# Kernel optimization log

Hardware: AMD Instinct MI355X
Metric: run time of the kernel (lower is better)

The kernel has to match this reference:

```python
import jax, jax.numpy as jnp
import numpy as np

SOFTMAX_SCALE = 0.5  # passed as scalar arg in the original op

def setup_inputs() -> dict:
    key = jax.random.key(0)
    ks = jax.random.split(key, 6)
    B, Sq, H, D, Smax = 8, 1, 32, 128, 4096
    q = jax.random.normal(ks[0], (B, Sq, H, D), dtype=jnp.float32)
    k = jax.random.normal(ks[1], (B, Sq, H, D), dtype=jnp.float32)
    v = jax.random.normal(ks[2], (B, Sq, H, D), dtype=jnp.float32)
    kcache = jax.random.normal(ks[3], (B, Smax, H, D), dtype=jnp.float32)
    vcache = jax.random.normal(ks[4], (B, Smax, H, D), dtype=jnp.float32)
    # current cache occupancy per batch; ensure seqlen + Sq <= Smax
    seqlen = jax.random.randint(ks[5], (B,), 0, Smax - Sq).astype(jnp.int32)
    return {"q": q, "k": k, "v": v, "kcache": kcache, "vcache": vcache, "seqlen": seqlen}

def reference(q, k, v, kcache, vcache, seqlen):
    # Semantics of flash_attn_with_kvcache: append k/v into the cache at
    # offset seqlen[b], then causally attend q over cache[: seqlen[b] + S_new].
    # Causal alignment is bottom-right: query i maps to key position
    # seqlen + S_new - S_q + i.
    B, Sq, H, D = q.shape
    Smax = kcache.shape[1]
    Snew = k.shape[1]
    pos_k = jnp.arange(Smax)          # [Smax]
    pos_q = jnp.arange(Sq)            # [Sq]

    def one_batch(qb, kb, vb, kcb, vcb, sl):
        # qb: [Sq,H,D]; kcb/vcb: [Smax,H,D]; sl: scalar int32
        kc = jax.lax.dynamic_update_slice(kcb, kb, (sl, 0, 0))
        vc = jax.lax.dynamic_update_slice(vcb, vb, (sl, 0, 0))
        scores = jnp.einsum('qhd,khd->hqk', qb, kc) * SOFTMAX_SCALE  # [H,Sq,Smax]
        kmax = sl + Snew - Sq + pos_q                                # [Sq]
        mask = pos_k[None, :] <= kmax[:, None]                       # [Sq,Smax]
        scores = jnp.where(mask[None, :, :], scores, -jnp.inf)
        p = jax.nn.softmax(scores, axis=-1)
        return jnp.einsum('hqk,khd->qhd', p, vc)                     # [Sq,H,D]

    return jax.vmap(one_batch)(q, k, v, kcache, vcache, seqlen)
```

## Files before the change

kernel.cpp:

```cpp
#include <hip/hip_runtime.h>
#include <math.h>

#define B_    8
#define H_    32
#define D_    128
#define SMAX_ 4096
#define SCALE 0.5f

__global__ __launch_bounds__(256, 4)
void attn_partial(const float* __restrict__ q,
                  const float* __restrict__ knew,
                  const float* __restrict__ vnew,
                  const float* __restrict__ kcache,
                  const float* __restrict__ vcache,
                  const int* __restrict__ seqlen,
                  float* __restrict__ ws,
                  float* __restrict__ out,
                  int nsplit, int chunk)
{
    const int blk   = blockIdx.x;
    const int split = blk % nsplit;
    const int bh    = blk / nsplit;
    const int h     = bh & (H_ - 1);
    const int b     = bh / H_;

    const int sl    = seqlen[b];
    const int total = sl + 1;
    const int cs    = split * chunk;
    const int ce    = min(cs + chunk, total);

    const int tid    = threadIdx.x;
    const int lane16 = tid & 15;
    const int gid    = tid >> 4;

    const int qbase = (b * H_ + h) * D_ + lane16 * 8;
    float qf[8];
    {
        float4 q0 = *(const float4*)(q + qbase);
        float4 q1 = *(const float4*)(q + qbase + 4);
        qf[0]=q0.x; qf[1]=q0.y; qf[2]=q0.z; qf[3]=q0.w;
        qf[4]=q1.x; qf[5]=q1.y; qf[6]=q1.z; qf[7]=q1.w;
    }

    float m = -1e30f, l = 0.f;
    float acc[8];
    #pragma unroll
    for (int j = 0; j < 8; ++j) acc[j] = 0.f;

    const size_t cbase = (size_t)b * SMAX_ * (H_ * D_) + (size_t)h * D_ + (size_t)(lane16 * 8);

    for (int p = cs + gid; p < ce; p += 16) {
        const float* kp;
        const float* vp;
        if (p == sl) {
            kp = knew + qbase;
            vp = vnew + qbase;
        } else {
            size_t off = cbase + (size_t)p * (H_ * D_);
            kp = kcache + off;
            vp = vcache + off;
        }
        float4 k0 = *(const float4*)(kp);
        float4 k1 = *(const float4*)(kp + 4);
        float4 v0 = *(const float4*)(vp);
        float4 v1 = *(const float4*)(vp + 4);

        float s = qf[0]*k0.x + qf[1]*k0.y + qf[2]*k0.z + qf[3]*k0.w
                + qf[4]*k1.x + qf[5]*k1.y + qf[6]*k1.z + qf[7]*k1.w;
        s += __shfl_xor(s, 1);
        s += __shfl_xor(s, 2);
        s += __shfl_xor(s, 4);
        s += __shfl_xor(s, 8);
        s *= SCALE;

        float mn = fmaxf(m, s);
        float sc = __expf(m - mn);
        float pr = __expf(s - mn);
        m = mn;
        l = l * sc + pr;
        acc[0] = fmaf(pr, v0.x, acc[0]*sc);
        acc[1] = fmaf(pr, v0.y, acc[1]*sc);
        acc[2] = fmaf(pr, v0.z, acc[2]*sc);
        acc[3] = fmaf(pr, v0.w, acc[3]*sc);
        acc[4] = fmaf(pr, v1.x, acc[4]*sc);
        acc[5] = fmaf(pr, v1.y, acc[5]*sc);
        acc[6] = fmaf(pr, v1.z, acc[6]*sc);
        acc[7] = fmaf(pr, v1.w, acc[7]*sc);
    }

    #pragma unroll
    for (int off = 16; off <= 32; off <<= 1) {
        float m2 = __shfl_xor(m, off);
        float l2 = __shfl_xor(l, off);
        float a2[8];
        #pragma unroll
        for (int j = 0; j < 8; ++j) a2[j] = __shfl_xor(acc[j], off);
        float mn = fmaxf(m, m2);
        float s1 = __expf(m - mn);
        float s2 = __expf(m2 - mn);
        l = l * s1 + l2 * s2;
        #pragma unroll
        for (int j = 0; j < 8; ++j) acc[j] = acc[j]*s1 + a2[j]*s2;
        m = mn;
    }

    __shared__ float sm_m[4];
    __shared__ float sm_l[4];
    __shared__ float sm_acc[4][D_];
    const int w    = tid >> 6;
    const int lane = tid & 63;
    if (lane < 16) {
        if (lane == 0) { sm_m[w] = m; sm_l[w] = l; }
        #pragma unroll
        for (int j = 0; j < 8; ++j) sm_acc[w][lane16*8 + j] = acc[j];
    }
    __syncthreads();

    if (tid < D_) {
        float m0 = sm_m[0], m1 = sm_m[1], m2 = sm_m[2], m3 = sm_m[3];
        float mt = fmaxf(fmaxf(m0, m1), fmaxf(m2, m3));
        float e0 = __expf(m0 - mt), e1 = __expf(m1 - mt);
        float e2 = __expf(m2 - mt), e3 = __expf(m3 - mt);
        float lt = sm_l[0]*e0 + sm_l[1]*e1 + sm_l[2]*e2 + sm_l[3]*e3;
        float a  = sm_acc[0][tid]*e0 + sm_acc[1][tid]*e1
                 + sm_acc[2][tid]*e2 + sm_acc[3][tid]*e3;
        if (nsplit == 1) {
            out[bh * D_ + tid] = a / lt;
        } else {
            float* wsp = ws + (size_t)blk * (D_ + 2);
            if (tid == 0) { wsp[0] = mt; wsp[1] = lt; }
            wsp[2 + tid] = a;
        }
    }
}

__global__ __launch_bounds__(128)
void attn_combine(const float* __restrict__ ws, float* __restrict__ out, int nsplit)
{
    const int bh = blockIdx.x;
    const int d  = threadIdx.x;
    const float* base = ws + (size_t)bh * nsplit * (D_ + 2);

    float mt = -1e30f;
    for (int s = 0; s < nsplit; ++s) mt = fmaxf(mt, base[(size_t)s * (D_ + 2)]);
    float lt = 0.f, a = 0.f;
    for (int s = 0; s < nsplit; ++s) {
        const float* p = base + (size_t)s * (D_ + 2);
        float e = __expf(p[0] - mt);
        lt += p[1] * e;
        a  += p[2 + d] * e;
    }
    out[bh * D_ + d] = a / lt;
}

extern "C" void kernel_launch(void* const* d_in, const int* in_sizes, int n_in,
                              void* d_out, int out_size, void* d_ws, size_t ws_size,
                              hipStream_t stream) {
    const float* q  = (const float*)d_in[0];
    const float* k  = (const float*)d_in[1];
    const float* v  = (const float*)d_in[2];
    const float* kc = (const float*)d_in[3];
    const float* vc = (const float*)d_in[4];
    const int*   sl = (const int*)d_in[5];
    float* out = (float*)d_out;
    float* ws  = (float*)d_ws;

    int nsplit = 16;
    while (nsplit > 1 &&
           (size_t)B_ * H_ * nsplit * (D_ + 2) * sizeof(float) > ws_size) {
        nsplit >>= 1;
    }
    const int chunk = (SMAX_ + nsplit - 1) / nsplit;
    const int nblk  = B_ * H_ * nsplit;

    attn_partial<<<nblk, 256, 0, stream>>>(q, k, v, kc, vc, sl, ws, out, nsplit, chunk);
    if (nsplit > 1) {
        attn_combine<<<B_ * H_, 128, 0, stream>>>(ws, out, nsplit);
    }
}
```

Measured before the change: 140.1 us.

## Map all heads into one block per batch split, processing full contiguous cache rows

Each block now handles one batch and one sequence split across all 32 heads, so each thread reads 16 contiguous floats and a block covers a full contiguous 16KB cache row per position instead of a 512B head slice. The split count rises to 128 with a rewritten combine kernel that uses shuffle reductions and handles empty splits. The main loop is unrolled by two positions with a shared max update, and the new-token branch is hoisted out of the loop. Possible costs are higher register pressure from 16-wide accumulators and a heavier combine pass, and the nsplit==1 direct-output path is removed, so the combine launch always runs.

New measurement: 196.7 us. 40.4% more time.

```diff
diff --git a/kernel.cpp b/kernel.cpp
--- a/kernel.cpp
+++ b/kernel.cpp
@@ -5,7 +5,9 @@
 #define H_    32
 #define D_    128
 #define SMAX_ 4096
+#define HD_   (H_ * D_)
 #define SCALE 0.5f
+#define PSTRIDE (D_ + 2)
 
 __global__ __launch_bounds__(256, 4)
 void attn_partial(const float* __restrict__ q,
@@ -15,142 +17,196 @@
                   const float* __restrict__ vcache,
                   const int* __restrict__ seqlen,
                   float* __restrict__ ws,
-                  float* __restrict__ out,
                   int nsplit, int chunk)
 {
     const int blk   = blockIdx.x;
     const int split = blk % nsplit;
-    const int bh    = blk / nsplit;
-    const int h     = bh & (H_ - 1);
-    const int b     = bh / H_;
+    const int b     = blk / nsplit;
+    const int tid   = threadIdx.x;
+    const int h     = tid >> 3;
+    const int ds    = (tid & 7) * 16;
 
     const int sl    = seqlen[b];
     const int total = sl + 1;
     const int cs    = split * chunk;
     const int ce    = min(cs + chunk, total);
 
-    const int tid    = threadIdx.x;
-    const int lane16 = tid & 15;
-    const int gid    = tid >> 4;
-
-    const int qbase = (b * H_ + h) * D_ + lane16 * 8;
-    float qf[8];
+    float* wsp = ws + (((size_t)b * nsplit + split) * H_ + h) * PSTRIDE;
+
+    if (cs >= ce) {
+        if ((tid & 7) == 0) { wsp[0] = -1e30f; wsp[1] = 0.f; }
+        return;
+    }
+
+    float qf[16];
     {
-        float4 q0 = *(const float4*)(q + qbase);
-        float4 q1 = *(const float4*)(q + qbase + 4);
-        qf[0]=q0.x; qf[1]=q0.y; qf[2]=q0.z; qf[3]=q0.w;
-        qf[4]=q1.x; qf[5]=q1.y; qf[6]=q1.z; qf[7]=q1.w;
+        const float* qp = q + (b * H_ + h) * D_ + ds;
+        float4 t0 = *(const float4*)(qp);
+        float4 t1 = *(const float4*)(qp + 4);
+        float4 t2 = *(const float4*)(qp + 8);
+        float4 t3 = *(const float4*)(qp + 12);
+        qf[0]=t0.x;  qf[1]=t0.y;  qf[2]=t0.z;  qf[3]=t0.w;
+        qf[4]=t1.x;  qf[5]=t1.y;  qf[6]=t1.z;  qf[7]=t1.w;
+        qf[8]=t2.x;  qf[9]=t2.y;  qf[10]=t2.z; qf[11]=t2.w;
+        qf[12]=t3.x; qf[13]=t3.y; qf[14]=t3.z; qf[15]=t3.w;
     }
 
     float m = -1e30f, l = 0.f;
-    float acc[8];
+    float acc[16];
     #pragma unroll
-    for (int j = 0; j < 8; ++j) acc[j] = 0.f;
-
-    const size_t cbase = (size_t)b * SMAX_ * (H_ * D_) + (size_t)h * D_ + (size_t)(lane16 * 8);
-
-    for (int p = cs + gid; p < ce; p += 16) {
-        const float* kp;
-        const float* vp;
-        if (p == sl) {
-            kp = knew + qbase;
-            vp = vnew + qbase;
-        } else {
-            size_t off = cbase + (size_t)p * (H_ * D_);
-            kp = kcache + off;
-            vp = vcache + off;
-        }
-        float4 k0 = *(const float4*)(kp);
-        float4 k1 = *(const float4*)(kp + 4);
-        float4 v0 = *(const float4*)(vp);
-        float4 v1 = *(const float4*)(vp + 4);
-
-        float s = qf[0]*k0.x + qf[1]*k0.y + qf[2]*k0.z + qf[3]*k0.w
-                + qf[4]*k1.x + qf[5]*k1.y + qf[6]*k1.z + qf[7]*k1.w;
-        s += __shfl_xor(s, 1);
-        s += __shfl_xor(s, 2);
-        s += __shfl_xor(s, 4);
-        s += __shfl_xor(s, 8);
-        s *= SCALE;
-
-        float mn = fmaxf(m, s);
-        float sc = __expf(m - mn);
-        float pr = __expf(s - mn);
+    for (int j = 0; j < 16; ++j) acc[j] = 0.f;
+
+    const float* kb = kcache + (size_t)b * SMAX_ * HD_ + tid * 16;
+    const float* vb = vcache + (size_t)b * SMAX_ * HD_ + tid * 16;
+
+#define STEP1(KP, VP) do {                                                    \
+    float4 k0 = *(const float4*)(KP);                                         \
+    float4 k1 = *(const float4*)((KP)+4);                                     \
+    float4 k2 = *(const float4*)((KP)+8);                                     \
+    float4 k3 = *(const float4*)((KP)+12);                                    \
+    float4 v0 = *(const float4*)(VP);                                         \
+    float4 v1 = *(const float4*)((VP)+4);                                     \
+    float4 v2 = *(const float4*)((VP)+8);                                     \
+    float4 v3 = *(const float4*)((VP)+12);                                    \
+    float s = qf[0]*k0.x+qf[1]*k0.y+qf[2]*k0.z+qf[3]*k0.w                     \
+            + qf[4]*k1.x+qf[5]*k1.y+qf[6]*k1.z+qf[7]*k1.w                     \
+            + qf[8]*k2.x+qf[9]*k2.y+qf[10]*k2.z+qf[11]*k2.w                   \
+            + qf[12]*k3.x+qf[13]*k3.y+qf[14]*k3.z+qf[15]*k3.w;                \
+    s += __shfl_xor(s, 1); s += __shfl_xor(s, 2); s += __shfl_xor(s, 4);      \
+    s *= SCALE;                                                               \
+    float mn = fmaxf(m, s);                                                   \
+    float sc = __expf(m - mn);                                                \
+    float pr = __expf(s - mn);                                                \
+    m = mn; l = l * sc + pr;                                                  \
+    acc[0]=fmaf(pr,v0.x,acc[0]*sc);  acc[1]=fmaf(pr,v0.y,acc[1]*sc);          \
+    acc[2]=fmaf(pr,v0.z,acc[2]*sc);  acc[3]=fmaf(pr,v0.w,acc[3]*sc);          \
+    acc[4]=fmaf(pr,v1.x,acc[4]*sc);  acc[5]=fmaf(pr,v1.y,acc[5]*sc);          \
+    acc[6]=fmaf(pr,v1.z,acc[6]*sc);  acc[7]=fmaf(pr,v1.w,acc[7]*sc);          \
+    acc[8]=fmaf(pr,v2.x,acc[8]*sc);  acc[9]=fmaf(pr,v2.y,acc[9]*sc);          \
+    acc[10]=fmaf(pr,v2.z,acc[10]*sc);acc[11]=fmaf(pr,v2.w,acc[11]*sc);        \
+    acc[12]=fmaf(pr,v3.x,acc[12]*sc);acc[13]=fmaf(pr,v3.y,acc[13]*sc);        \
+    acc[14]=fmaf(pr,v3.z,acc[14]*sc);acc[15]=fmaf(pr,v3.w,acc[15]*sc);        \
+} while (0)
+
+    const int pend = min(ce, sl);
+    int p = cs;
+    for (; p + 2 <= pend; p += 2) {
+        const float* kp0 = kb + (size_t)p * HD_;
+        const float* vp0 = vb + (size_t)p * HD_;
+        const float* kp1 = kp0 + HD_;
+        const float* vp1 = vp0 + HD_;
+        float4 a0 = *(const float4*)(kp0);
+        float4 a1 = *(const float4*)(kp0+4);
+        float4 a2 = *(const float4*)(kp0+8);
+        float4 a3 = *(const float4*)(kp0+12);
+        float4 b0 = *(const float4*)(kp1);
+        float4 b1 = *(const float4*)(kp1+4);
+        float4 b2 = *(const float4*)(kp1+8);
+        float4 b3 = *(const float4*)(kp1+12);
+        float4 u0 = *(const float4*)(vp0);
+        float4 u1 = *(const float4*)(vp0+4);
+        float4 u2 = *(const float4*)(vp0+8);
+        float4 u3 = *(const float4*)(vp0+12);
+        float4 w0 = *(const float4*)(vp1);
+        float4 w1 = *(const float4*)(vp1+4);
+        float4 w2 = *(const float4*)(vp1+8);
+        float4 w3 = *(const float4*)(vp1+12);
+
+        float s0 = qf[0]*a0.x+qf[1]*a0.y+qf[2]*a0.z+qf[3]*a0.w
+                 + qf[4]*a1.x+qf[5]*a1.y+qf[6]*a1.z+qf[7]*a1.w
+                 + qf[8]*a2.x+qf[9]*a2.y+qf[10]*a2.z+qf[11]*a2.w
+                 + qf[12]*a3.x+qf[13]*a3.y+qf[14]*a3.z+qf[15]*a3.w;
+        float s1 = qf[0]*b0.x+qf[1]*b0.y+qf[2]*b0.z+qf[3]*b0.w
+                 + qf[4]*b1.x+qf[5]*b1.y+qf[6]*b1.z+qf[7]*b1.w
+                 + qf[8]*b2.x+qf[9]*b2.y+qf[10]*b2.z+qf[11]*b2.w
+                 + qf[12]*b3.x+qf[13]*b3.y+qf[14]*b3.z+qf[15]*b3.w;
+        s0 += __shfl_xor(s0, 1); s0 += __shfl_xor(s0, 2); s0 += __shfl_xor(s0, 4);
+        s1 += __shfl_xor(s1, 1); s1 += __shfl_xor(s1, 2); s1 += __shfl_xor(s1, 4);
+        s0 *= SCALE; s1 *= SCALE;
+
+        float mn  = fmaxf(m, fmaxf(s0, s1));
+        float sc  = __expf(m - mn);
+        float pr0 = __expf(s0 - mn);
+        float pr1 = __expf(s1 - mn);
         m = mn;
-        l = l * sc + pr;
-        acc[0] = fmaf(pr, v0.x, acc[0]*sc);
-        acc[1] = fmaf(pr, v0.y, acc[1]*sc);
-        acc[2] = fmaf(pr, v0.z, acc[2]*sc);
-        acc[3] = fmaf(pr, v0.w, acc[3]*sc);
-        acc[4] = fmaf(pr, v1.x, acc[4]*sc);
-        acc[5] = fmaf(pr, v1.y, acc[5]*sc);
-        acc[6] = fmaf(pr, v1.z, acc[6]*sc);
-        acc[7] = fmaf(pr, v1.w, acc[7]*sc);
-    }
-
-    #pragma unroll
-    for (int off = 16; off <= 32; off <<= 1) {
-        float m2 = __shfl_xor(m, off);
-        float l2 = __shfl_xor(l, off);
-        float a2[8];
-        #pragma unroll
-        for (int j = 0; j < 8; ++j) a2[j] = __shfl_xor(acc[j], off);
-        float mn = fmaxf(m, m2);
-        float s1 = __expf(m - mn);
-        float s2 = __expf(m2 - mn);
-        l = l * s1 + l2 * s2;
-        #pragma unroll
-        for (int j = 0; j < 8; ++j) acc[j] = acc[j]*s1 + a2[j]*s2;
-        m = mn;
-    }
-
-    __shared__ float sm_m[4];
-    __shared__ float sm_l[4];
-    __shared__ float sm_acc[4][D_];
-    const int w    = tid >> 6;
-    const int lane = tid & 63;
-    if (lane < 16) {
-        if (lane == 0) { sm_m[w] = m; sm_l[w] = l; }
-        #pragma unroll
-        for (int j = 0; j < 8; ++j) sm_acc[w][lane16*8 + j] = acc[j];
-    }
-    __syncthreads();
-
-    if (tid < D_) {
-        float m0 = sm_m[0], m1 = sm_m[1], m2 = sm_m[2], m3 = sm_m[3];
-        float mt = fmaxf(fmaxf(m0, m1), fmaxf(m2, m3));
-        float e0 = __expf(m0 - mt), e1 = __expf(m1 - mt);
-        float e2 = __expf(m2 - mt), e3 = __expf(m3 - mt);
-        float lt = sm_l[0]*e0 + sm_l[1]*e1 + sm_l[2]*e2 + sm_l[3]*e3;
-        float a  = sm_acc[0][tid]*e0 + sm_acc[1][tid]*e1
-                 + sm_acc[2][tid]*e2 + sm_acc[3][tid]*e3;
-        if (nsplit == 1) {
-            out[bh * D_ + tid] = a / lt;
-        } else {
-            float* wsp = ws + (size_t)blk * (D_ + 2);
-            if (tid == 0) { wsp[0] = mt; wsp[1] = lt; }
-            wsp[2 + tid] = a;
-        }
-    }
+        l = l * sc + pr0 + pr1;
+        acc[0] = fmaf(pr1,w0.x, fmaf(pr0,u0.x, acc[0] *sc));
+        acc[1] = fmaf(pr1,w0.y, fmaf(pr0,u0.y, acc[1] *sc));
+        acc[2] = fmaf(pr1,w0.z, fmaf(pr0,u0.z, acc[2] *sc));
+        acc[3] = fmaf(pr1,w0.w, fmaf(pr0,u0.w, acc[3] *sc));
+        acc[4] = fmaf(pr1,w1.x, fmaf(pr0,u1.x, acc[4] *sc));
+        acc[5] = fmaf(pr1,w1.y, fmaf(pr0,u1.y, acc[5] *sc));
+        acc[6] = fmaf(pr1,w1.z, fmaf(pr0,u1.z, acc[6] *sc));
+        acc[7] = fmaf(pr1,w1.w, fmaf(pr0,u1.w, acc[7] *sc));
+        acc[8] = fmaf(pr1,w2.x, fmaf(pr0,u2.x, acc[8] *sc));
+        acc[9] = fmaf(pr1,w2.y, fmaf(pr0,u2.y, acc[9] *sc));
+        acc[10]= fmaf(pr1,w2.z, fmaf(pr0,u2.z, acc[10]*sc));
+        acc[11]= fmaf(pr1,w2.w, fmaf(pr0,u2.w, acc[11]*sc));
+        acc[12]= fmaf(pr1,w3.x, fmaf(pr0,u3.x, acc[12]*sc));
+        acc[13]= fmaf(pr1,w3.y, fmaf(pr0,u3.y, acc[13]*sc));
+        acc[14]= fmaf(pr1,w3.z, fmaf(pr0,u3.z, acc[14]*sc));
+        acc[15]= fmaf(pr1,w3.w, fmaf(pr0,u3.w, acc[15]*sc));
+    }
+    for (; p < pend; ++p) {
+        const float* kp = kb + (size_t)p * HD_;
+        const float* vp = vb + (size_t)p * HD_;
+        STEP1(kp, vp);
+    }
+    if (sl >= cs && sl < ce) {
+        const float* kp = knew + (size_t)b * HD_ + tid * 16;
+        const float* vp = vnew + (size_t)b * HD_ + tid * 16;
+        STEP1(kp, vp);
+    }
+#undef STEP1
+
+    if ((tid & 7) == 0) { wsp[0] = m; wsp[1] = l; }
+    float* op = wsp + 2 + ds;
+    *(float4*)(op)      = make_float4(acc[0],  acc[1],  acc[2],  acc[3]);
+    *(float4*)(op + 4)  = make_float4(acc[4],  acc[5],  acc[6],  acc[7]);
+    *(float4*)(op + 8)  = make_float4(acc[8],  acc[9],  acc[10], acc[11]);
+    *(float4*)(op + 12) = make_float4(acc[12], acc[13], acc[14], acc[15]);
 }
 
 __global__ __launch_bounds__(128)
 void attn_combine(const float* __restrict__ ws, float* __restrict__ out, int nsplit)
 {
     const int bh = blockIdx.x;
-    const int d  = threadIdx.x;
-    const float* base = ws + (size_t)bh * nsplit * (D_ + 2);
-
-    float mt = -1e30f;
-    for (int s = 0; s < nsplit; ++s) mt = fmaxf(mt, base[(size_t)s * (D_ + 2)]);
-    float lt = 0.f, a = 0.f;
+    const int b  = bh >> 5;
+    const int h  = bh & (H_ - 1);
+    const int t  = threadIdx.x;
+
+    __shared__ float sm_e[128];
+    __shared__ float sm_w[2];
+
+    float m_s = -1e30f, l_s = 0.f;
+    const float* ps = ws + (((size_t)b * nsplit + t) * H_ + h) * PSTRIDE;
+    if (t < nsplit) { m_s = ps[0]; l_s = ps[1]; }
+
+    float mx = m_s;
+    #pragma unroll
+    for (int off = 1; off < 64; off <<= 1) mx = fmaxf(mx, __shfl_xor(mx, off));
+    if ((t & 63) == 0) sm_w[t >> 6] = mx;
+    __syncthreads();
+    const float mt = fmaxf(sm_w[0], sm_w[1]);
+    __syncthreads();
+
+    const float e = (l_s > 0.f) ? __expf(m_s - mt) : 0.f;
+    sm_e[t] = e;
+    float le = l_s * e;
+    #pragma unroll
+    for (int off = 1; off < 64; off <<= 1) le += __shfl_xor(le, off);
+    if ((t & 63) == 0) sm_w[t >> 6] = le;
+    __syncthreads();
+    const float lt = sm_w[0] + sm_w[1];
+
+    const float* ab = ws + ((size_t)b * nsplit * H_ + h) * PSTRIDE + 2 + t;
+    const size_t sstride = (size_t)H_ * PSTRIDE;
+    float a = 0.f;
+    #pragma unroll 8
     for (int s = 0; s < nsplit; ++s) {
-        const float* p = base + (size_t)s * (D_ + 2);
-        float e = __expf(p[0] - mt);
-        lt += p[1] * e;
-        a  += p[2 + d] * e;
-    }
-    out[bh * D_ + d] = a / lt;
+        a += sm_e[s] * ab[(size_t)s * sstride];
+    }
+    out[bh * D_ + t] = a / lt;
 }
 
 extern "C" void kernel_launch(void* const* d_in, const int* in_sizes, int n_in,
@@ -165,16 +221,13 @@
     float* out = (float*)d_out;
     float* ws  = (float*)d_ws;
 
-    int nsplit = 16;
+    int nsplit = 128;
     while (nsplit > 1 &&
-           (size_t)B_ * H_ * nsplit * (D_ + 2) * sizeof(float) > ws_size) {
+           (size_t)B_ * nsplit * H_ * PSTRIDE * sizeof(float) > ws_size) {
         nsplit >>= 1;
     }
-    const int chunk = (SMAX_ + nsplit - 1) / nsplit;
-    const int nblk  = B_ * H_ * nsplit;
-
-    attn_partial<<<nblk, 256, 0, stream>>>(q, k, v, kc, vc, sl, ws, out, nsplit, chunk);
-    if (nsplit > 1) {
-        attn_combine<<<B_ * H_, 128, 0, stream>>>(ws, out, nsplit);
-    }
+    const int chunk = SMAX_ / nsplit;
+
+    attn_partial<<<B_ * nsplit, 256, 0, stream>>>(q, k, v, kc, vc, sl, ws, nsplit, chunk);
+    attn_combine<<<B_ * H_, 128, 0, stream>>>(ws, out, nsplit);
 }
```

## Use contiguous per-group KV ranges, nontemporal loads, 2-way unroll, fixed splits

Applied to the files above, without the earlier changes.

Each 16-thread group now scans a contiguous 16-position sub-range of its 256-position chunk instead of striding by 16. The main loop handles two positions per iteration with nontemporal vector loads. The new-token check is moved out of the loop, and the split count is hardcoded so the launch and combine code lose their runtime parameters. The aim is more loads in flight, less per-position branching, and no cache pollution from streaming KV data. The cost is that the workspace size is no longer checked, and groups whose ranges fall past seqlen now sit idle.

Result: slower. 162.1 us (+15.7%).

```diff
diff --git a/kernel.cpp b/kernel.cpp
--- a/kernel.cpp
+++ b/kernel.cpp
@@ -5,7 +5,17 @@
 #define H_    32
 #define D_    128
 #define SMAX_ 4096
+#define HD_   (H_ * D_)
 #define SCALE 0.5f
+#define PSTRIDE (D_ + 2)
+#define NSPLIT 16
+#define CHUNK  256
+
+typedef float vfloat4 __attribute__((ext_vector_type(4)));
+
+__device__ __forceinline__ vfloat4 ntload4(const float* p) {
+    return __builtin_nontemporal_load((const vfloat4*)p);
+}
 
 __global__ __launch_bounds__(256, 4)
 void attn_partial(const float* __restrict__ q,
@@ -15,19 +25,18 @@
                   const float* __restrict__ vcache,
                   const int* __restrict__ seqlen,
                   float* __restrict__ ws,
-                  float* __restrict__ out,
-                  int nsplit, int chunk)
+                  float* __restrict__ out)
 {
     const int blk   = blockIdx.x;
-    const int split = blk % nsplit;
-    const int bh    = blk / nsplit;
+    const int split = blk & (NSPLIT - 1);
+    const int bh    = blk / NSPLIT;
     const int h     = bh & (H_ - 1);
     const int b     = bh / H_;
 
     const int sl    = seqlen[b];
     const int total = sl + 1;
-    const int cs    = split * chunk;
-    const int ce    = min(cs + chunk, total);
+    const int cs    = split * CHUNK;
+    const int ce    = min(cs + CHUNK, total);
 
     const int tid    = threadIdx.x;
     const int lane16 = tid & 15;
@@ -47,46 +56,82 @@
     #pragma unroll
     for (int j = 0; j < 8; ++j) acc[j] = 0.f;
 
-    const size_t cbase = (size_t)b * SMAX_ * (H_ * D_) + (size_t)h * D_ + (size_t)(lane16 * 8);
-
-    for (int p = cs + gid; p < ce; p += 16) {
-        const float* kp;
-        const float* vp;
-        if (p == sl) {
-            kp = knew + qbase;
-            vp = vnew + qbase;
-        } else {
-            size_t off = cbase + (size_t)p * (H_ * D_);
-            kp = kcache + off;
-            vp = vcache + off;
-        }
-        float4 k0 = *(const float4*)(kp);
-        float4 k1 = *(const float4*)(kp + 4);
-        float4 v0 = *(const float4*)(vp);
-        float4 v1 = *(const float4*)(vp + 4);
-
-        float s = qf[0]*k0.x + qf[1]*k0.y + qf[2]*k0.z + qf[3]*k0.w
-                + qf[4]*k1.x + qf[5]*k1.y + qf[6]*k1.z + qf[7]*k1.w;
-        s += __shfl_xor(s, 1);
-        s += __shfl_xor(s, 2);
-        s += __shfl_xor(s, 4);
-        s += __shfl_xor(s, 8);
-        s *= SCALE;
-
-        float mn = fmaxf(m, s);
-        float sc = __expf(m - mn);
-        float pr = __expf(s - mn);
+    const size_t cbase = (size_t)b * SMAX_ * HD_ + (size_t)h * D_ + (size_t)(lane16 * 8);
+
+#define STEP1(KP, VP) do {                                                    \
+    vfloat4 k0 = ntload4(KP);                                                 \
+    vfloat4 k1 = ntload4((KP)+4);                                             \
+    vfloat4 v0 = ntload4(VP);                                                 \
+    vfloat4 v1 = ntload4((VP)+4);                                             \
+    float s = qf[0]*k0.x+qf[1]*k0.y+qf[2]*k0.z+qf[3]*k0.w                     \
+            + qf[4]*k1.x+qf[5]*k1.y+qf[6]*k1.z+qf[7]*k1.w;                    \
+    s += __shfl_xor(s, 1); s += __shfl_xor(s, 2);                             \
+    s += __shfl_xor(s, 4); s += __shfl_xor(s, 8);                             \
+    s *= SCALE;                                                               \
+    float mn = fmaxf(m, s);                                                   \
+    float sc = __expf(m - mn);                                                \
+    float pr = __expf(s - mn);                                                \
+    m = mn; l = l * sc + pr;                                                  \
+    acc[0]=fmaf(pr,v0.x,acc[0]*sc); acc[1]=fmaf(pr,v0.y,acc[1]*sc);           \
+    acc[2]=fmaf(pr,v0.z,acc[2]*sc); acc[3]=fmaf(pr,v0.w,acc[3]*sc);           \
+    acc[4]=fmaf(pr,v1.x,acc[4]*sc); acc[5]=fmaf(pr,v1.y,acc[5]*sc);           \
+    acc[6]=fmaf(pr,v1.z,acc[6]*sc); acc[7]=fmaf(pr,v1.w,acc[7]*sc);           \
+} while (0)
+
+    const int gs   = cs + gid * (CHUNK / 16);
+    const int ge   = min(gs + (CHUNK / 16), ce);
+    const int pend = min(ge, sl);
+
+    const float* kp = kcache + cbase + (size_t)gs * HD_;
+    const float* vp = vcache + cbase + (size_t)gs * HD_;
+
+    int p = gs;
+    for (; p + 2 <= pend; p += 2) {
+        vfloat4 a0 = ntload4(kp);
+        vfloat4 a1 = ntload4(kp + 4);
+        vfloat4 b0 = ntload4(kp + HD_);
+        vfloat4 b1 = ntload4(kp + HD_ + 4);
+        vfloat4 u0 = ntload4(vp);
+        vfloat4 u1 = ntload4(vp + 4);
+        vfloat4 w0 = ntload4(vp + HD_);
+        vfloat4 w1 = ntload4(vp + HD_ + 4);
+
+        float s0 = qf[0]*a0.x+qf[1]*a0.y+qf[2]*a0.z+qf[3]*a0.w
+                 + qf[4]*a1.x+qf[5]*a1.y+qf[6]*a1.z+qf[7]*a1.w;
+        float s1 = qf[0]*b0.x+qf[1]*b0.y+qf[2]*b0.z+qf[3]*b0.w
+                 + qf[4]*b1.x+qf[5]*b1.y+qf[6]*b1.z+qf[7]*b1.w;
+        s0 += __shfl_xor(s0, 1); s0 += __shfl_xor(s0, 2);
+        s0 += __shfl_xor(s0, 4); s0 += __shfl_xor(s0, 8);
+        s1 += __shfl_xor(s1, 1); s1 += __shfl_xor(s1, 2);
+        s1 += __shfl_xor(s1, 4); s1 += __shfl_xor(s1, 8);
+        s0 *= SCALE; s1 *= SCALE;
+
+        float mn  = fmaxf(m, fmaxf(s0, s1));
+        float sc  = __expf(m - mn);
+        float pr0 = __expf(s0 - mn);
+        float pr1 = __expf(s1 - mn);
         m = mn;
-        l = l * sc + pr;
-        acc[0] = fmaf(pr, v0.x, acc[0]*sc);
-        acc[1] = fmaf(pr, v0.y, acc[1]*sc);
-        acc[2] = fmaf(pr, v0.z, acc[2]*sc);
-        acc[3] = fmaf(pr, v0.w, acc[3]*sc);
-        acc[4] = fmaf(pr, v1.x, acc[4]*sc);
-        acc[5] = fmaf(pr, v1.y, acc[5]*sc);
-        acc[6] = fmaf(pr, v1.z, acc[6]*sc);
-        acc[7] = fmaf(pr, v1.w, acc[7]*sc);
-    }
+        l = l * sc + pr0 + pr1;
+        acc[0] = fmaf(pr1,w0.x, fmaf(pr0,u0.x, acc[0]*sc));
+        acc[1] = fmaf(pr1,w0.y, fmaf(pr0,u0.y, acc[1]*sc));
+        acc[2] = fmaf(pr1,w0.z, fmaf(pr0,u0.z, acc[2]*sc));
+        acc[3] = fmaf(pr1,w0.w, fmaf(pr0,u0.w, acc[3]*sc));
+        acc[4] = fmaf(pr1,w1.x, fmaf(pr0,u1.x, acc[4]*sc));
+        acc[5] = fmaf(pr1,w1.y, fmaf(pr0,u1.y, acc[5]*sc));
+        acc[6] = fmaf(pr1,w1.z, fmaf(pr0,u1.z, acc[6]*sc));
+        acc[7] = fmaf(pr1,w1.w, fmaf(pr0,u1.w, acc[7]*sc));
+        kp += 2 * HD_;
+        vp += 2 * HD_;
+    }
+    if (p < pend) {
+        STEP1(kp, vp);
+    }
+    if (sl >= gs && sl < ge) {
+        const float* kn = knew + qbase;
+        const float* vn = vnew + qbase;
+        STEP1(kn, vn);
+    }
+#undef STEP1
 
     #pragma unroll
     for (int off = 16; off <= 32; off <<= 1) {
@@ -124,30 +169,29 @@
         float lt = sm_l[0]*e0 + sm_l[1]*e1 + sm_l[2]*e2 + sm_l[3]*e3;
         float a  = sm_acc[0][tid]*e0 + sm_acc[1][tid]*e1
                  + sm_acc[2][tid]*e2 + sm_acc[3][tid]*e3;
-        if (nsplit == 1) {
-            out[bh * D_ + tid] = a / lt;
-        } else {
-            float* wsp = ws + (size_t)blk * (D_ + 2);
-            if (tid == 0) { wsp[0] = mt; wsp[1] = lt; }
-            wsp[2 + tid] = a;
-        }
+        float* wsp = ws + (size_t)blk * PSTRIDE;
+        if (tid == 0) { wsp[0] = mt; wsp[1] = lt; }
+        wsp[2 + tid] = a;
     }
 }
 
 __global__ __launch_bounds__(128)
-void attn_combine(const float* __restrict__ ws, float* __restrict__ out, int nsplit)
+void attn_combine(const float* __restrict__ ws, float* __restrict__ out)
 {
     const int bh = blockIdx.x;
     const int d  = threadIdx.x;
-    const float* base = ws + (size_t)bh * nsplit * (D_ + 2);
+    const float* base = ws + (size_t)bh * NSPLIT * PSTRIDE;
 
     float mt = -1e30f;
-    for (int s = 0; s < nsplit; ++s) mt = fmaxf(mt, base[(size_t)s * (D_ + 2)]);
+    #pragma unroll
+    for (int s = 0; s < NSPLIT; ++s) mt = fmaxf(mt, base[(size_t)s * PSTRIDE]);
     float lt = 0.f, a = 0.f;
-    for (int s = 0; s < nsplit; ++s) {
-        const float* p = base + (size_t)s * (D_ + 2);
-        float e = __expf(p[0] - mt);
-        lt += p[1] * e;
+    #pragma unroll
+    for (int s = 0; s < NSPLIT; ++s) {
+        const float* p = base + (size_t)s * PSTRIDE;
+        float ls = p[1];
+        float e  = (ls > 0.f) ? __expf(p[0] - mt) : 0.f;
+        lt += ls * e;
         a  += p[2 + d] * e;
     }
     out[bh * D_ + d] = a / lt;
@@ -165,16 +209,6 @@
     float* out = (float*)d_out;
     float* ws  = (float*)d_ws;
 
-    int nsplit = 16;
-    while (nsplit > 1 &&
-           (size_t)B_ * H_ * nsplit * (D_ + 2) * sizeof(float) > ws_size) {
-        nsplit >>= 1;
-    }
-    const int chunk = (SMAX_ + nsplit - 1) / nsplit;
-    const int nblk  = B_ * H_ * nsplit;
-
-    attn_partial<<<nblk, 256, 0, stream>>>(q, k, v, kc, vc, sl, ws, out, nsplit, chunk);
-    if (nsplit > 1) {
-        attn_combine<<<B_ * H_, 128, 0, stream>>>(ws, out, nsplit);
-    }
-}
+    attn_partial<<<B_ * H_ * NSPLIT, 256, 0, stream>>>(q, k, v, kc, vc, sl, ws, out);
+    attn_combine<<<B_ * H_, 128, 0, stream>>>(ws, out);
+}
```
